# Optimization experiments

Hardware: AMD Instinct MI355X
Metric: run time of the kernel (lower is better)

## Reference

```python
import jax, jax.numpy as jnp
import numpy as np
import math

D = 1024
H = 16
HD = D // H


def setup_inputs() -> dict:
    key = jax.random.key(0)
    ks = jax.random.split(key, 12)
    B, L = 2, 2048
    s = 1.0 / math.sqrt(D)
    inp = {
        "q": jax.random.normal(ks[0], (B, L, D), jnp.float32),
        "k": jax.random.normal(ks[1], (B, L, D), jnp.float32),
        "v": jax.random.normal(ks[2], (B, L, D), jnp.float32),
        "Wq": jax.random.normal(ks[3], (D, D), jnp.float32) * s,
        "bq": jnp.zeros((D,), jnp.float32),
        "Wk": jax.random.normal(ks[4], (D, D), jnp.float32) * s,
        "bk": jnp.zeros((D,), jnp.float32),
        "Wv": jax.random.normal(ks[5], (D, D), jnp.float32) * s,
        "bv": jnp.zeros((D,), jnp.float32),
        "Wo": jax.random.normal(ks[6], (D, D), jnp.float32) * s,
        "bo": jnp.zeros((D,), jnp.float32),
        "P": jax.random.normal(ks[7], (H, H), jnp.float32),  # logit_proj_pre
    }
    return inp


def _split_heads(x, B, L):
    # [B,L,D] -> [B,H,L,HD]
    return x.reshape(B, L, H, HD).transpose(0, 2, 1, 3)


def reference(q, k, v, Wq, bq, Wk, bk, Wv, bv, Wo, bo, P):
    B, L, _ = q.shape
    qh = _split_heads(q @ Wq.T + bq, B, L)
    kh = _split_heads(k @ Wk.T + bk, B, L)
    vh = _split_heads(v @ Wv.T + bv, B, L)
    # raw per-head logits [B,H,L,L]
    logits = jnp.einsum("bhld,bhmd->bhlm", qh, kh) / math.sqrt(HD)
    # talking-heads mixing across heads (pre-softmax)
    logits = jnp.einsum("bhlm,hg->bglm", logits, P)
    attn = jax.nn.softmax(logits, axis=-1)
    out = jnp.einsum("bhlm,bhmd->bhld", attn, vh)  # [B,H,L,HD]
    out = out.transpose(0, 2, 1, 3).reshape(B, L, D)
    return out @ Wo.T + bo
```

## Files before the change

kernel.cpp:

```cpp
#include <hip/hip_runtime.h>

#define D_  1024
#define H_  16
#define HD_ 64
#define L_  2048
#define B_  2
#define M_  (B_*L_)

typedef float f32x4  __attribute__((ext_vector_type(4)));
typedef short bf16x4 __attribute__((ext_vector_type(4)));
typedef short bf16x8 __attribute__((ext_vector_type(8)));

#define SRAW_PITCH 18
#define SRAW_SLAB  (16 * SRAW_PITCH)
#define VS_PITCH   36

__device__ __forceinline__ float bf2f(short s) {
    return __uint_as_float(((unsigned int)(unsigned short)s) << 16);
}
__device__ __forceinline__ short f2bf(float f) {
    unsigned u = __float_as_uint(f);
    unsigned r = (u + 0x7FFFu + ((u >> 16) & 1u)) >> 16;
    return (short)r;
}
__device__ __forceinline__ void block_sync() {
    asm volatile("s_waitcnt lgkmcnt(0)" ::: "memory");
    __builtin_amdgcn_sched_barrier(0);
    __builtin_amdgcn_s_barrier();
    __builtin_amdgcn_sched_barrier(0);
}

__global__ __launch_bounds__(256) void proj_mfma(
    const float* __restrict__ q, const float* __restrict__ k, const float* __restrict__ v,
    const float* __restrict__ Wq, const float* __restrict__ bq,
    const float* __restrict__ Wk, const float* __restrict__ bk,
    const float* __restrict__ Wv, const float* __restrict__ bv,
    short* __restrict__ qh, short* __restrict__ qlo,
    short* __restrict__ kh, short* __restrict__ vht)
{
    const int z = blockIdx.z;
    const float* X    = (z == 0) ? q  : (z == 1) ? k  : v;
    const float* W    = (z == 0) ? Wq : (z == 1) ? Wk : Wv;
    const float* bias = (z == 0) ? bq : (z == 1) ? bk : bv;

    __shared__ short Ws[128][40];
    __shared__ short Xs[128][40];

    const int tid  = threadIdx.x;
    const int w    = tid >> 6, lane = tid & 63;
    const int l16  = lane & 15, qq = lane >> 4;
    const int m0   = blockIdx.x * 128;
    const int n0   = blockIdx.y * 128;
    const int ar0  = 64 * (w & 1);
    const int br0  = 64 * (w >> 1);

    f32x4 acc[4][4] = {};

    for (int k0 = 0; k0 < D_; k0 += 32) {
        #pragma unroll
        for (int i = 0; i < 4; ++i) {
            int fidx = i * 256 + tid;
            int r = fidx >> 3, c = fidx & 7;
            float4 wv4 = *(const float4*)(W + (size_t)(n0 + r) * D_ + k0 + c * 4);
            float4 xv4 = *(const float4*)(X + (size_t)(m0 + r) * D_ + k0 + c * 4);
            bf16x4 wb = { f2bf(wv4.x), f2bf(wv4.y), f2bf(wv4.z), f2bf(wv4.w) };
            bf16x4 xb = { f2bf(xv4.x), f2bf(xv4.y), f2bf(xv4.z), f2bf(xv4.w) };
            *(bf16x4*)&Ws[r][c * 4] = wb;
            *(bf16x4*)&Xs[r][c * 4] = xb;
        }
        __syncthreads();
        bf16x8 af[4], bfv[4];
        #pragma unroll
        for (int i = 0; i < 4; ++i) {
            const short* Ab = (z < 2) ? &Ws[ar0 + 16 * i + l16][qq * 8]
                                      : &Xs[ar0 + 16 * i + l16][qq * 8];
            const short* Bb = (z < 2) ? &Xs[br0 + 16 * i + l16][qq * 8]
                                      : &Ws[br0 + 16 * i + l16][qq * 8];
            af[i]  = *(const bf16x8*)Ab;
            bfv[i] = *(const bf16x8*)Bb;
        }
        #pragma unroll
        for (int i = 0; i < 4; ++i)
            #pragma unroll
            for (int j = 0; j < 4; ++j)
                acc[i][j] = __builtin_amdgcn_mfma_f32_16x16x32_bf16(af[i], bfv[j], acc[i][j], 0, 0, 0);
        __syncthreads();
    }

    if (z < 2) {
        #pragma unroll
        for (int i = 0; i < 4; ++i) {
            int nb = n0 + ar0 + 16 * i + qq * 4;
            float4 b4 = *(const float4*)(bias + nb);
            int h = nb >> 6, hd = nb & 63;
            #pragma unroll
            for (int j = 0; j < 4; ++j) {
                int m = m0 + br0 + 16 * j + l16;
                int bb = m >> 11, l = m & (L_ - 1);
                size_t o = ((((size_t)bb * H_ + h) * L_) + l) * HD_ + hd;
                f32x4 c = acc[i][j];
                float v0 = c[0] + b4.x, v1 = c[1] + b4.y, v2 = c[2] + b4.z, v3 = c[3] + b4.w;
                bf16x4 hi = { f2bf(v0), f2bf(v1), f2bf(v2), f2bf(v3) };
                if (z == 0) {
                    *(bf16x4*)&qh[o] = hi;
                    bf16x4 lo = { f2bf(v0 - bf2f(hi[0])), f2bf(v1 - bf2f(hi[1])),
                                  f2bf(v2 - bf2f(hi[2])), f2bf(v3 - bf2f(hi[3])) };
                    *(bf16x4*)&qlo[o] = lo;
                } else {
                    *(bf16x4*)&kh[o] = hi;
                }
            }
        }
    } else {
        #pragma unroll
        for (int i = 0; i < 4; ++i) {
            int mb = m0 + ar0 + 16 * i + qq * 4;
            int bb = mb >> 11, lb = mb & (L_ - 1);
            #pragma unroll
            for (int j = 0; j < 4; ++j) {
                int n = n0 + br0 + 16 * j + l16;
                int h = n >> 6, hd = n & 63;
                float bn = bias[n];
                size_t o = (((size_t)bb * H_ + h) * HD_ + hd) * (size_t)L_ + lb;
                f32x4 c = acc[i][j];
                bf16x4 ov = { f2bf(c[0] + bn), f2bf(c[1] + bn), f2bf(c[2] + bn), f2bf(c[3] + bn) };
                *(bf16x4*)&vht[o] = ov;
            }
        }
    }
}

__global__ __launch_bounds__(512, 2) void attn_mfma(
    const short* __restrict__ qh, const short* __restrict__ qlo,
    const short* __restrict__ kh, const short* __restrict__ vht,
    const float* __restrict__ P, short* __restrict__ attn_out)
{
    __shared__ __align__(16) float Sraw0[16 * SRAW_SLAB];
    __shared__ __align__(16) float Sraw1[16 * SRAW_SLAB];
    __shared__ __align__(16) float Smix[16 * SRAW_SLAB];
    __shared__ __align__(16) short Vslab[8][2 * 64 * VS_PITCH];
    __shared__ float PmS[256];

    const int tid  = threadIdx.x;
    const int n    = blockIdx.x;
    const int b    = (n >> 2) & 1;
    const int l0   = ((n >> 3) * 4 + (n & 3)) * 16;
    const int w    = tid >> 6, lane = tid & 63;
    const int l16  = lane & 15, qq = lane >> 4;
    const size_t hb = (size_t)b * H_;

    bf16x8 qf[2][2][2];
    #pragma unroll
    for (int hh = 0; hh < 2; ++hh)
        #pragma unroll
        for (int kc = 0; kc < 2; ++kc) {
            size_t off = ((hb + 2 * w + hh) * L_ + l0 + l16) * HD_ + kc * 32 + qq * 8;
            qf[hh][kc][0] = *(const bf16x8*)(qh  + off);
            qf[hh][kc][1] = *(const bf16x8*)(qlo + off);
        }

    int vgi_[4], vd_[4];
    const int vc = lane & 1;
    #pragma unroll
    for (int i = 0; i < 4; ++i) {
        int vrow = i * 32 + (lane >> 1);
        vgi_[i] = vrow >> 6;
        vd_[i]  = vrow & 63;
    }
    int vwoff[4];
    #pragma unroll
    for (int i = 0; i < 4; ++i)
        vwoff[i] = vgi_[i] * (64 * VS_PITCH) + vd_[i] * VS_PITCH + vc * 8;

    bf16x8 kA[2][2], kB[2][2], vA[4], vB[4];
    #pragma unroll
    for (int hh = 0; hh < 2; ++hh)
        #pragma unroll
        for (int kc = 0; kc < 2; ++kc) {
            kA[hh][kc] = *(const bf16x8*)(kh + ((hb + 2 * w + hh) * L_ + 0  + l16) * HD_ + kc * 32 + qq * 8);
            kB[hh][kc] = *(const bf16x8*)(kh + ((hb + 2 * w + hh) * L_ + 16 + l16) * HD_ + kc * 32 + qq * 8);
        }
    #pragma unroll
    for (int i = 0; i < 4; ++i) {
        vA[i] = *(const bf16x8*)(vht + ((hb + 2 * w + vgi_[i]) * HD_ + vd_[i]) * (size_t)L_ + 0  + vc * 8);
        vB[i] = *(const bf16x8*)(vht + ((hb + 2 * w + vgi_[i]) * HD_ + vd_[i]) * (size_t)L_ + 16 + vc * 8);
    }

    if (tid < 256) PmS[tid] = P[tid] * 0.125f;

    f32x4 acc[2][4];
    #pragma unroll
    for (int dt = 0; dt < 4; ++dt) { acc[0][dt] = (f32x4){0.f,0.f,0.f,0.f}; acc[1][dt] = (f32x4){0.f,0.f,0.f,0.f}; }
    float mrun0 = 0.f, mrun1 = 0.f, srun0 = 0.f, srun1 = 0.f;

    auto qkt = [&](bf16x8 (&kr)[2][2], float* sb) {
        #pragma unroll
        for (int hh = 0; hh < 2; ++hh) {
            f32x4 s = (f32x4){0.f,0.f,0.f,0.f};
            s = __builtin_amdgcn_mfma_f32_16x16x32_bf16(kr[hh][0], qf[hh][0][0], s, 0, 0, 0);
            s = __builtin_amdgcn_mfma_f32_16x16x32_bf16(kr[hh][0], qf[hh][0][1], s, 0, 0, 0);
            s = __builtin_amdgcn_mfma_f32_16x16x32_bf16(kr[hh][1], qf[hh][1][0], s, 0, 0, 0);
            s = __builtin_amdgcn_mfma_f32_16x16x32_bf16(kr[hh][1], qf[hh][1][1], s, 0, 0, 0);
            float* sp = sb + ((2 * w + hh) * 16 + l16) * SRAW_PITCH + qq * 4;
            *(float2*)sp       = make_float2(s[0], s[1]);
            *(float2*)(sp + 2) = make_float2(s[2], s[3]);
        }
    };

    qkt(kA, Sraw0);
    block_sync();

    bf16x4 PAhi, PAlo;
    {
        float p0 = PmS[(qq * 4 + 0) * 16 + l16];
        float p1 = PmS[(qq * 4 + 1) * 16 + l16];
        float p2 = PmS[(qq * 4 + 2) * 16 + l16];
        float p3 = PmS[(qq * 4 + 3) * 16 + l16];
        PAhi = (bf16x4){ f2bf(p0), f2bf(p1), f2bf(p2), f2bf(p3) };
        PAlo = (bf16x4){ f2bf(p0 - bf2f(PAhi[0])), f2bf(p1 - bf2f(PAhi[1])),
                         f2bf(p2 - bf2f(PAhi[2])), f2bf(p3 - bf2f(PAhi[3])) };
    }

    auto mixmfma = [&](const float* sb) {
        #pragma unroll
        for (int mi = 0; mi < 2; ++mi) {
            const int m = 2 * w + mi;
            float sv0 = sb[(qq * 4 + 0) * SRAW_SLAB + l16 * SRAW_PITCH + m];
            float sv1 = sb[(qq * 4 + 1) * SRAW_SLAB + l16 * SRAW_PITCH + m];
            float sv2 = sb[(qq * 4 + 2) * SRAW_SLAB + l16 * SRAW_PITCH + m];
            float sv3 = sb[(qq * 4 + 3) * SRAW_SLAB + l16 * SRAW_PITCH + m];
            bf16x4 bhi = { f2bf(sv0), f2bf(sv1), f2bf(sv2), f2bf(sv3) };
            bf16x4 blo = { f2bf(sv0 - bf2f(bhi[0])), f2bf(sv1 - bf2f(bhi[1])),
                           f2bf(sv2 - bf2f(bhi[2])), f2bf(sv3 - bf2f(bhi[3])) };
            f32x4 c = (f32x4){0.f, 0.f, 0.f, 0.f};
            c = __builtin_amdgcn_mfma_f32_16x16x16bf16_1k(PAhi, bhi, c, 0, 0, 0);
            c = __builtin_amdgcn_mfma_f32_16x16x16bf16_1k(PAhi, blo, c, 0, 0, 0);
            c = __builtin_amdgcn_mfma_f32_16x16x16bf16_1k(PAlo, bhi, c, 0, 0, 0);
            float* sp = Smix + m * SRAW_SLAB + l16 * SRAW_PITCH + qq * 4;
            *(float2*)sp       = make_float2(c[0], c[1]);
            *(float2*)(sp + 2) = make_float2(c[2], c[3]);
        }
    };

    auto body = [&](const float* sb, float* sbo, bf16x8 (&vstage)[4], bf16x8 (&kqk)[2][2],
                    bf16x8 (&kld)[2][2], bf16x8 (&vld)[4], int tnext) {
        #pragma unroll
        for (int i = 0; i < 4; ++i) {
            bf16x4 wlo = { vstage[i][0], vstage[i][1], vstage[i][2], vstage[i][3] };
            bf16x4 whi = { vstage[i][4], vstage[i][5], vstage[i][6], vstage[i][7] };
            *(bf16x4*)&Vslab[w][vwoff[i]]     = wlo;
            *(bf16x4*)&Vslab[w][vwoff[i] + 4] = whi;
        }
        {
            const int mn = tnext * 16;
            #pragma unroll
            for (int hh = 0; hh < 2; ++hh)
                #pragma unroll
                for (int kc = 0; kc < 2; ++kc)
                    kld[hh][kc] = *(const bf16x8*)(kh + ((hb + 2 * w + hh) * L_ + mn + l16) * HD_ + kc * 32 + qq * 8);
            #pragma unroll
            for (int i = 0; i < 4; ++i)
                vld[i] = *(const bf16x8*)(vht + ((hb + 2 * w + vgi_[i]) * HD_ + vd_[i]) * (size_t)L_ + mn + vc * 8);
        }
        mixmfma(sb);
        block_sync();
        float sx0[4], sx1[4];
        #pragma unroll
        for (int j = 0; j < 4; ++j) {
            const float* mp = Smix + (qq * 4 + j) * SRAW_SLAB + l16 * SRAW_PITCH;
            sx0[j] = mp[2 * w];
            sx1[j] = mp[2 * w + 1];
        }
        float e00 = __expf(sx0[0] - mrun0), e01 = __expf(sx0[1] - mrun0);
        float e02 = __expf(sx0[2] - mrun0), e03 = __expf(sx0[3] - mrun0);
        float e10 = __expf(sx1[0] - mrun1), e11 = __expf(sx1[1] - mrun1);
        float e12 = __expf(sx1[2] - mrun1), e13 = __expf(sx1[3] - mrun1);
        bf16x4 pf0 = { f2bf(e00), f2bf(e01), f2bf(e02), f2bf(e03) };
        bf16x4 pf1 = { f2bf(e10), f2bf(e11), f2bf(e12), f2bf(e13) };
        float t0 = fmaxf(fmaxf(sx0[0], sx0[1]), fmaxf(sx0[2], sx0[3]));
        float t1 = fmaxf(fmaxf(sx1[0], sx1[1]), fmaxf(sx1[2], sx1[3]));
        t0 = fmaxf(t0, __shfl_xor(t0, 16)); t0 = fmaxf(t0, __shfl_xor(t0, 32));
        t1 = fmaxf(t1, __shfl_xor(t1, 16)); t1 = fmaxf(t1, __shfl_xor(t1, 32));
        float ps0 = e00 + e01 + e02 + e03, ps1 = e10 + e11 + e12 + e13;
        ps0 += __shfl_xor(ps0, 16); ps0 += __shfl_xor(ps0, 32);
        ps1 += __shfl_xor(ps1, 16); ps1 += __shfl_xor(ps1, 32);
        #pragma unroll
        for (int i = 0; i < 2; ++i) {
            bf16x4 pf = i ? pf1 : pf0;
            #pragma unroll
            for (int dt = 0; dt < 4; ++dt) {
                bf16x4 afr = *(const bf16x4*)&Vslab[w][i * (64 * VS_PITCH) + (dt * 16 + l16) * VS_PITCH + qq * 4];
                acc[i][dt] = __builtin_amdgcn_mfma_f32_16x16x16bf16_1k(afr, pf, acc[i][dt], 0, 0, 0);
            }
        }
        qkt(kqk, sbo);
        float mnew0 = fmaxf(mrun0, t0), mnew1 = fmaxf(mrun1, t1);
        float corr0 = __expf(mrun0 - mnew0), corr1 = __expf(mrun1 - mnew1);
        srun0 = (srun0 + ps0) * corr0; srun1 = (srun1 + ps1) * corr1;
        acc[0][0] *= corr0; acc[0][1] *= corr0; acc[0][2] *= corr0; acc[0][3] *= corr0;
        acc[1][0] *= corr1; acc[1][1] *= corr1; acc[1][2] *= corr1; acc[1][3] *= corr1;
        mrun0 = mnew0; mrun1 = mnew1;
        block_sync();
    };

    for (int itp = 0; itp < 64; ++itp) {
        const int t0 = 2 * itp;
        body(Sraw0, Sraw1, vA, kB, kA, vA, (t0 + 2) & 127);
        body(Sraw1, Sraw0, vB, kA, kB, vB, (t0 + 3) & 127);
    }

    float inv0 = 1.f / srun0, inv1 = 1.f / srun1;
    #pragma unroll
    for (int i = 0; i < 2; ++i) {
        float inv = i ? inv1 : inv0;
        #pragma unroll
        for (int dt = 0; dt < 4; ++dt) {
            f32x4 a = acc[i][dt];
            bf16x4 ov = { f2bf(a[0] * inv), f2bf(a[1] * inv), f2bf(a[2] * inv), f2bf(a[3] * inv) };
            *(bf16x4*)(attn_out + ((size_t)(b * L_ + l0 + l16)) * D_ + (2 * w + i) * 64 + dt * 16 + qq * 4) = ov;
        }
    }
}

__global__ __launch_bounds__(256) void out_mfma(
    const short* __restrict__ attn, const float* __restrict__ Wo,
    const float* __restrict__ bo, float* __restrict__ out)
{
    __shared__ short Ws[128][40];
    __shared__ short Xs[128][40];

    const int tid = threadIdx.x;
    const int w = tid >> 6, lane = tid & 63;
    const int l16 = lane & 15, qq = lane >> 4;
    const int m0 = blockIdx.x * 128;
    const int n0 = blockIdx.y * 128;
    const int ar0 = 64 * (w & 1);
    const int br0 = 64 * (w >> 1);

    f32x4 acc[4][4] = {};

    for (int k0 = 0; k0 < D_; k0 += 32) {
        #pragma unroll
        for (int i = 0; i < 4; ++i) {
            int fidx = i * 256 + tid;
            int r = fidx >> 3, c = fidx & 7;
            float4 wv4 = *(const float4*)(Wo + (size_t)(n0 + r) * D_ + k0 + c * 4);
            bf16x4 wb = { f2bf(wv4.x), f2bf(wv4.y), f2bf(wv4.z), f2bf(wv4.w) };
            *(bf16x4*)&Ws[r][c * 4] = wb;
        }
        #pragma unroll
        for (int i = 0; i < 2; ++i) {
            int cidx = i * 256 + tid;
            int r = cidx >> 2, c = cidx & 3;
            bf16x8 xv = *(const bf16x8*)(attn + (size_t)(m0 + r) * D_ + k0 + c * 8);
            *(bf16x8*)&Xs[r][c * 8] = xv;
        }
        __syncthreads();
        bf16x8 af[4], bfv[4];
        #pragma unroll
        for (int i = 0; i < 4; ++i) {
            af[i]  = *(const bf16x8*)&Ws[ar0 + 16 * i + l16][qq * 8];
            bfv[i] = *(const bf16x8*)&Xs[br0 + 16 * i + l16][qq * 8];
        }
        #pragma unroll
        for (int i = 0; i < 4; ++i)
            #pragma unroll
            for (int j = 0; j < 4; ++j)
                acc[i][j] = __builtin_amdgcn_mfma_f32_16x16x32_bf16(af[i], bfv[j], acc[i][j], 0, 0, 0);
        __syncthreads();
    }

    #pragma unroll
    for (int i = 0; i < 4; ++i) {
        int nb = n0 + ar0 + 16 * i + qq * 4;
        float4 b4 = *(const float4*)(bo + nb);
        #pragma unroll
        for (int j = 0; j < 4; ++j) {
            int m = m0 + br0 + 16 * j + l16;
            f32x4 c = acc[i][j];
            float4 ov = make_float4(c[0] + b4.x, c[1] + b4.y, c[2] + b4.z, c[3] + b4.w);
            *(float4*)&out[(size_t)m * D_ + nb] = ov;
        }
    }
}

extern "C" void kernel_launch(void* const* d_in, const int* in_sizes, int n_in,
                              void* d_out, int out_size, void* d_ws, size_t ws_size,
                              hipStream_t stream) {
    const float* q  = (const float*)d_in[0];
    const float* k  = (const float*)d_in[1];
    const float* v  = (const float*)d_in[2];
    const float* Wq = (const float*)d_in[3];
    const float* bq = (const float*)d_in[4];
    const float* Wk = (const float*)d_in[5];
    const float* bk = (const float*)d_in[6];
    const float* Wv = (const float*)d_in[7];
    const float* bv = (const float*)d_in[8];
    const float* Wo = (const float*)d_in[9];
    const float* bo = (const float*)d_in[10];
    const float* P  = (const float*)d_in[11];
    float* out = (float*)d_out;

    char* ws = (char*)d_ws;
    short* qh   = (short*)(ws);
    short* qlo  = (short*)(ws + (size_t)8 * 1024 * 1024);
    short* kh   = (short*)(ws + (size_t)16 * 1024 * 1024);
    short* vht  = (short*)(ws + (size_t)24 * 1024 * 1024);
    short* attn = (short*)(ws + (size_t)32 * 1024 * 1024);

    proj_mfma<<<dim3(M_ / 128, D_ / 128, 3), 256, 0, stream>>>(
        q, k, v, Wq, bq, Wk, bk, Wv, bv, qh, qlo, kh, vht);
    attn_mfma<<<dim3(256), 512, 0, stream>>>(qh, qlo, kh, vht, P, attn);
    out_mfma<<<dim3(M_ / 128, D_ / 128), 256, 0, stream>>>(attn, Wo, bo, out);
}
```

Measured before the change: 408.1 us.

## Process two key tiles per attention iteration to halve block barriers

The attention loop now handles two 16-key tiles per iteration. A second Smix buffer lets both tiles be head-mixed before a single barrier, and one online-softmax max/sum update covers both tiles. K and V fragments are prefetched two tiles ahead through small load lambdas. This halves the number of block-wide barriers and exposes more independent MFMA/exp work, at the cost of extra LDS (another Smix slab) and higher register pressure.

```diff
diff --git a/kernel.cpp b/kernel.cpp
--- a/kernel.cpp
+++ b/kernel.cpp
@@ -135,9 +135,10 @@
     const short* __restrict__ kh, const short* __restrict__ vht,
     const float* __restrict__ P, short* __restrict__ attn_out)
 {
-    __shared__ __align__(16) float Sraw0[16 * SRAW_SLAB];
-    __shared__ __align__(16) float Sraw1[16 * SRAW_SLAB];
-    __shared__ __align__(16) float Smix[16 * SRAW_SLAB];
+    __shared__ __align__(16) float SrawA[16 * SRAW_SLAB];
+    __shared__ __align__(16) float SrawB[16 * SRAW_SLAB];
+    __shared__ __align__(16) float SmixA[16 * SRAW_SLAB];
+    __shared__ __align__(16) float SmixB[16 * SRAW_SLAB];
     __shared__ __align__(16) short Vslab[8][2 * 64 * VS_PITCH];
     __shared__ float PmS[256];
 
@@ -172,19 +173,24 @@
     for (int i = 0; i < 4; ++i)
         vwoff[i] = vgi_[i] * (64 * VS_PITCH) + vd_[i] * VS_PITCH + vc * 8;
 
-    bf16x8 kA[2][2], kB[2][2], vA[4], vB[4];
-    #pragma unroll
-    for (int hh = 0; hh < 2; ++hh)
-        #pragma unroll
-        for (int kc = 0; kc < 2; ++kc) {
-            kA[hh][kc] = *(const bf16x8*)(kh + ((hb + 2 * w + hh) * L_ + 0  + l16) * HD_ + kc * 32 + qq * 8);
-            kB[hh][kc] = *(const bf16x8*)(kh + ((hb + 2 * w + hh) * L_ + 16 + l16) * HD_ + kc * 32 + qq * 8);
-        }
-    #pragma unroll
-    for (int i = 0; i < 4; ++i) {
-        vA[i] = *(const bf16x8*)(vht + ((hb + 2 * w + vgi_[i]) * HD_ + vd_[i]) * (size_t)L_ + 0  + vc * 8);
-        vB[i] = *(const bf16x8*)(vht + ((hb + 2 * w + vgi_[i]) * HD_ + vd_[i]) * (size_t)L_ + 16 + vc * 8);
-    }
+    auto kload = [&](int tile, bf16x8 (&kdst)[2][2]) {
+        const int mn = (tile & 127) * 16;
+        #pragma unroll
+        for (int hh = 0; hh < 2; ++hh)
+            #pragma unroll
+            for (int kc = 0; kc < 2; ++kc)
+                kdst[hh][kc] = *(const bf16x8*)(kh + ((hb + 2 * w + hh) * L_ + mn + l16) * HD_ + kc * 32 + qq * 8);
+    };
+    auto vload = [&](int tile, bf16x8 (&vdst)[4]) {
+        const int mn = (tile & 127) * 16;
+        #pragma unroll
+        for (int i = 0; i < 4; ++i)
+            vdst[i] = *(const bf16x8*)(vht + ((hb + 2 * w + vgi_[i]) * HD_ + vd_[i]) * (size_t)L_ + mn + vc * 8);
+    };
+
+    bf16x8 kPa[2][2], kPb[2][2], vsta[4], vstb[4];
+    kload(0, kPa); kload(1, kPb);
+    vload(0, vsta); vload(1, vstb);
 
     if (tid < 256) PmS[tid] = P[tid] * 0.125f;
 
@@ -207,8 +213,10 @@
         }
     };
 
-    qkt(kA, Sraw0);
+    qkt(kPa, SrawA);
+    qkt(kPb, SrawB);
     block_sync();
+    kload(2, kPa); kload(3, kPb);
 
     bf16x4 PAhi, PAlo;
     {
@@ -221,7 +229,7 @@
                          f2bf(p2 - bf2f(PAhi[2])), f2bf(p3 - bf2f(PAhi[3])) };
     }
 
-    auto mixmfma = [&](const float* sb) {
+    auto mixmfma = [&](const float* sb, float* sm) {
         #pragma unroll
         for (int mi = 0; mi < 2; ++mi) {
             const int m = 2 * w + mi;
@@ -236,54 +244,20 @@
             c = __builtin_amdgcn_mfma_f32_16x16x16bf16_1k(PAhi, bhi, c, 0, 0, 0);
             c = __builtin_amdgcn_mfma_f32_16x16x16bf16_1k(PAhi, blo, c, 0, 0, 0);
             c = __builtin_amdgcn_mfma_f32_16x16x16bf16_1k(PAlo, bhi, c, 0, 0, 0);
-            float* sp = Smix + m * SRAW_SLAB + l16 * SRAW_PITCH + qq * 4;
+            float* sp = sm + m * SRAW_SLAB + l16 * SRAW_PITCH + qq * 4;
             *(float2*)sp       = make_float2(c[0], c[1]);
             *(float2*)(sp + 2) = make_float2(c[2], c[3]);
         }
     };
 
-    auto body = [&](const float* sb, float* sbo, bf16x8 (&vstage)[4], bf16x8 (&kqk)[2][2],
-                    bf16x8 (&kld)[2][2], bf16x8 (&vld)[4], int tnext) {
-        #pragma unroll
-        for (int i = 0; i < 4; ++i) {
-            bf16x4 wlo = { vstage[i][0], vstage[i][1], vstage[i][2], vstage[i][3] };
-            bf16x4 whi = { vstage[i][4], vstage[i][5], vstage[i][6], vstage[i][7] };
+    auto stage_pv = [&](bf16x8 (&vst)[4], bf16x4 pf0, bf16x4 pf1) {
+        #pragma unroll
+        for (int i = 0; i < 4; ++i) {
+            bf16x4 wlo = { vst[i][0], vst[i][1], vst[i][2], vst[i][3] };
+            bf16x4 whi = { vst[i][4], vst[i][5], vst[i][6], vst[i][7] };
             *(bf16x4*)&Vslab[w][vwoff[i]]     = wlo;
             *(bf16x4*)&Vslab[w][vwoff[i] + 4] = whi;
         }
-        {
-            const int mn = tnext * 16;
-            #pragma unroll
-            for (int hh = 0; hh < 2; ++hh)
-                #pragma unroll
-                for (int kc = 0; kc < 2; ++kc)
-                    kld[hh][kc] = *(const bf16x8*)(kh + ((hb + 2 * w + hh) * L_ + mn + l16) * HD_ + kc * 32 + qq * 8);
-            #pragma unroll
-            for (int i = 0; i < 4; ++i)
-                vld[i] = *(const bf16x8*)(vht + ((hb + 2 * w + vgi_[i]) * HD_ + vd_[i]) * (size_t)L_ + mn + vc * 8);
-        }
-        mixmfma(sb);
-        block_sync();
-        float sx0[4], sx1[4];
-        #pragma unroll
-        for (int j = 0; j < 4; ++j) {
-            const float* mp = Smix + (qq * 4 + j) * SRAW_SLAB + l16 * SRAW_PITCH;
-            sx0[j] = mp[2 * w];
-            sx1[j] = mp[2 * w + 1];
-        }
-        float e00 = __expf(sx0[0] - mrun0), e01 = __expf(sx0[1] - mrun0);
-        float e02 = __expf(sx0[2] - mrun0), e03 = __expf(sx0[3] - mrun0);
-        float e10 = __expf(sx1[0] - mrun1), e11 = __expf(sx1[1] - mrun1);
-        float e12 = __expf(sx1[2] - mrun1), e13 = __expf(sx1[3] - mrun1);
-        bf16x4 pf0 = { f2bf(e00), f2bf(e01), f2bf(e02), f2bf(e03) };
-        bf16x4 pf1 = { f2bf(e10), f2bf(e11), f2bf(e12), f2bf(e13) };
-        float t0 = fmaxf(fmaxf(sx0[0], sx0[1]), fmaxf(sx0[2], sx0[3]));
-        float t1 = fmaxf(fmaxf(sx1[0], sx1[1]), fmaxf(sx1[2], sx1[3]));
-        t0 = fmaxf(t0, __shfl_xor(t0, 16)); t0 = fmaxf(t0, __shfl_xor(t0, 32));
-        t1 = fmaxf(t1, __shfl_xor(t1, 16)); t1 = fmaxf(t1, __shfl_xor(t1, 32));
-        float ps0 = e00 + e01 + e02 + e03, ps1 = e10 + e11 + e12 + e13;
-        ps0 += __shfl_xor(ps0, 16); ps0 += __shfl_xor(ps0, 32);
-        ps1 += __shfl_xor(ps1, 16); ps1 += __shfl_xor(ps1, 32);
         #pragma unroll
         for (int i = 0; i < 2; ++i) {
             bf16x4 pf = i ? pf1 : pf0;
@@ -293,7 +267,50 @@
                 acc[i][dt] = __builtin_amdgcn_mfma_f32_16x16x16bf16_1k(afr, pf, acc[i][dt], 0, 0, 0);
             }
         }
-        qkt(kqk, sbo);
+    };
+
+    for (int t = 0; t < 64; ++t) {
+        mixmfma(SrawA, SmixA);
+        mixmfma(SrawB, SmixB);
+        block_sync();
+        float sxA0[4], sxA1[4], sxB0[4], sxB1[4];
+        #pragma unroll
+        for (int j = 0; j < 4; ++j) {
+            const float* mpA = SmixA + (qq * 4 + j) * SRAW_SLAB + l16 * SRAW_PITCH;
+            const float* mpB = SmixB + (qq * 4 + j) * SRAW_SLAB + l16 * SRAW_PITCH;
+            sxA0[j] = mpA[2 * w]; sxA1[j] = mpA[2 * w + 1];
+            sxB0[j] = mpB[2 * w]; sxB1[j] = mpB[2 * w + 1];
+        }
+        float eA00 = __expf(sxA0[0] - mrun0), eA01 = __expf(sxA0[1] - mrun0);
+        float eA02 = __expf(sxA0[2] - mrun0), eA03 = __expf(sxA0[3] - mrun0);
+        float eA10 = __expf(sxA1[0] - mrun1), eA11 = __expf(sxA1[1] - mrun1);
+        float eA12 = __expf(sxA1[2] - mrun1), eA13 = __expf(sxA1[3] - mrun1);
+        float eB00 = __expf(sxB0[0] - mrun0), eB01 = __expf(sxB0[1] - mrun0);
+        float eB02 = __expf(sxB0[2] - mrun0), eB03 = __expf(sxB0[3] - mrun0);
+        float eB10 = __expf(sxB1[0] - mrun1), eB11 = __expf(sxB1[1] - mrun1);
+        float eB12 = __expf(sxB1[2] - mrun1), eB13 = __expf(sxB1[3] - mrun1);
+        bf16x4 pfA0 = { f2bf(eA00), f2bf(eA01), f2bf(eA02), f2bf(eA03) };
+        bf16x4 pfA1 = { f2bf(eA10), f2bf(eA11), f2bf(eA12), f2bf(eA13) };
+        bf16x4 pfB0 = { f2bf(eB00), f2bf(eB01), f2bf(eB02), f2bf(eB03) };
+        bf16x4 pfB1 = { f2bf(eB10), f2bf(eB11), f2bf(eB12), f2bf(eB13) };
+        float t0 = fmaxf(fmaxf(fmaxf(sxA0[0], sxA0[1]), fmaxf(sxA0[2], sxA0[3])),
+                         fmaxf(fmaxf(sxB0[0], sxB0[1]), fmaxf(sxB0[2], sxB0[3])));
+        float t1 = fmaxf(fmaxf(fmaxf(sxA1[0], sxA1[1]), fmaxf(sxA1[2], sxA1[3])),
+                         fmaxf(fmaxf(sxB1[0], sxB1[1]), fmaxf(sxB1[2], sxB1[3])));
+        t0 = fmaxf(t0, __shfl_xor(t0, 16)); t0 = fmaxf(t0, __shfl_xor(t0, 32));
+        t1 = fmaxf(t1, __shfl_xor(t1, 16)); t1 = fmaxf(t1, __shfl_xor(t1, 32));
+        float ps0 = (eA00 + eA01 + eA02 + eA03) + (eB00 + eB01 + eB02 + eB03);
+        float ps1 = (eA10 + eA11 + eA12 + eA13) + (eB10 + eB11 + eB12 + eB13);
+        ps0 += __shfl_xor(ps0, 16); ps0 += __shfl_xor(ps0, 32);
+        ps1 += __shfl_xor(ps1, 16); ps1 += __shfl_xor(ps1, 32);
+        stage_pv(vsta, pfA0, pfA1);
+        vload(2 * t + 2, vsta);
+        stage_pv(vstb, pfB0, pfB1);
+        vload(2 * t + 3, vstb);
+        qkt(kPa, SrawA);
+        qkt(kPb, SrawB);
+        kload(2 * t + 4, kPa);
+        kload(2 * t + 5, kPb);
         float mnew0 = fmaxf(mrun0, t0), mnew1 = fmaxf(mrun1, t1);
         float corr0 = __expf(mrun0 - mnew0), corr1 = __expf(mrun1 - mnew1);
         srun0 = (srun0 + ps0) * corr0; srun1 = (srun1 + ps1) * corr1;
@@ -301,12 +318,6 @@
         acc[1][0] *= corr1; acc[1][1] *= corr1; acc[1][2] *= corr1; acc[1][3] *= corr1;
         mrun0 = mnew0; mrun1 = mnew1;
         block_sync();
-    };
-
-    for (int itp = 0; itp < 64; ++itp) {
-        const int t0 = 2 * itp;
-        body(Sraw0, Sraw1, vA, kB, kA, vA, (t0 + 2) & 127);
-        body(Sraw1, Sraw0, vB, kA, kB, vB, (t0 + 3) & 127);
     }
 
     float inv0 = 1.f / srun0, inv1 = 1.f / srun1;
```

Measured after the change: 403.9 us. Within noise of the previous version (-1.0%).

## Split attention KV range across two blocks and merge partial softmax results

Applied to the files above, without the earlier changes.

The attention kernel now splits the 2048-key range into two halves, so twice as many blocks (512) are launched, each handling 64 tiles. Each block writes fp32 partial accumulators and running max/sum to workspace, and a new merge kernel combines them with a log-sum-exp rescale. The main loop is restructured around a single Sraw buffer, with K/V prefetch reordered and a smaller V slab pitch, and the occupancy hint is raised to 4 blocks. The aim is better CU occupancy across the GPU, at the cost of extra global traffic for partials and one more launch; it falls back to the old path if the workspace is too small.

```diff
diff --git a/kernel.cpp b/kernel.cpp
--- a/kernel.cpp
+++ b/kernel.cpp
@@ -13,7 +13,7 @@
 
 #define SRAW_PITCH 18
 #define SRAW_SLAB  (16 * SRAW_PITCH)
-#define VS_PITCH   36
+#define VS_PITCH   20
 
 __device__ __forceinline__ float bf2f(short s) {
     return __uint_as_float(((unsigned int)(unsigned short)s) << 16);
@@ -130,21 +130,24 @@
     }
 }
 
-__global__ __launch_bounds__(512, 2) void attn_mfma(
+__global__ __launch_bounds__(512, 4) void attn_mfma(
     const short* __restrict__ qh, const short* __restrict__ qlo,
     const short* __restrict__ kh, const short* __restrict__ vht,
-    const float* __restrict__ P, short* __restrict__ attn_out)
+    const float* __restrict__ P, short* __restrict__ attn_out,
+    float* __restrict__ pacc, float* __restrict__ pms, int ntiles)
 {
-    __shared__ __align__(16) float Sraw0[16 * SRAW_SLAB];
-    __shared__ __align__(16) float Sraw1[16 * SRAW_SLAB];
+    __shared__ __align__(16) float Sraw[16 * SRAW_SLAB];
     __shared__ __align__(16) float Smix[16 * SRAW_SLAB];
     __shared__ __align__(16) short Vslab[8][2 * 64 * VS_PITCH];
     __shared__ float PmS[256];
 
     const int tid  = threadIdx.x;
     const int n    = blockIdx.x;
-    const int b    = (n >> 2) & 1;
-    const int l0   = ((n >> 3) * 4 + (n & 3)) * 16;
+    const int half = n >> 8;
+    const int inr  = n & 255;
+    const int b    = (inr >> 2) & 1;
+    const int l0   = ((inr >> 3) * 4 + (inr & 3)) * 16;
+    const int tb   = half * ntiles;
     const int w    = tid >> 6, lane = tid & 63;
     const int l16  = lane & 15, qq = lane >> 4;
     const size_t hb = (size_t)b * H_;
@@ -172,19 +175,23 @@
     for (int i = 0; i < 4; ++i)
         vwoff[i] = vgi_[i] * (64 * VS_PITCH) + vd_[i] * VS_PITCH + vc * 8;
 
-    bf16x8 kA[2][2], kB[2][2], vA[4], vB[4];
-    #pragma unroll
-    for (int hh = 0; hh < 2; ++hh)
-        #pragma unroll
-        for (int kc = 0; kc < 2; ++kc) {
-            kA[hh][kc] = *(const bf16x8*)(kh + ((hb + 2 * w + hh) * L_ + 0  + l16) * HD_ + kc * 32 + qq * 8);
-            kB[hh][kc] = *(const bf16x8*)(kh + ((hb + 2 * w + hh) * L_ + 16 + l16) * HD_ + kc * 32 + qq * 8);
-        }
-    #pragma unroll
-    for (int i = 0; i < 4; ++i) {
-        vA[i] = *(const bf16x8*)(vht + ((hb + 2 * w + vgi_[i]) * HD_ + vd_[i]) * (size_t)L_ + 0  + vc * 8);
-        vB[i] = *(const bf16x8*)(vht + ((hb + 2 * w + vgi_[i]) * HD_ + vd_[i]) * (size_t)L_ + 16 + vc * 8);
-    }
+    auto kload = [&](int tile, bf16x8 (&kdst)[2][2]) {
+        const int mn = (tile & 127) * 16;
+        #pragma unroll
+        for (int hh = 0; hh < 2; ++hh)
+            #pragma unroll
+            for (int kc = 0; kc < 2; ++kc)
+                kdst[hh][kc] = *(const bf16x8*)(kh + ((hb + 2 * w + hh) * L_ + mn + l16) * HD_ + kc * 32 + qq * 8);
+    };
+    auto vload = [&](int tile, bf16x8 (&vdst)[4]) {
+        const int mn = (tile & 127) * 16;
+        #pragma unroll
+        for (int i = 0; i < 4; ++i)
+            vdst[i] = *(const bf16x8*)(vht + ((hb + 2 * w + vgi_[i]) * HD_ + vd_[i]) * (size_t)L_ + mn + vc * 8);
+    };
+
+    bf16x8 kP[2][2], vst[4];
+    kload(tb, kP); vload(tb, vst);
 
     if (tid < 256) PmS[tid] = P[tid] * 0.125f;
 
@@ -207,8 +214,9 @@
         }
     };
 
-    qkt(kA, Sraw0);
+    qkt(kP, Sraw);
     block_sync();
+    kload(tb + 1, kP);
 
     bf16x4 PAhi, PAlo;
     {
@@ -221,14 +229,14 @@
                          f2bf(p2 - bf2f(PAhi[2])), f2bf(p3 - bf2f(PAhi[3])) };
     }
 
-    auto mixmfma = [&](const float* sb) {
+    for (int t = 0; t < ntiles; ++t) {
         #pragma unroll
         for (int mi = 0; mi < 2; ++mi) {
             const int m = 2 * w + mi;
-            float sv0 = sb[(qq * 4 + 0) * SRAW_SLAB + l16 * SRAW_PITCH + m];
-            float sv1 = sb[(qq * 4 + 1) * SRAW_SLAB + l16 * SRAW_PITCH + m];
-            float sv2 = sb[(qq * 4 + 2) * SRAW_SLAB + l16 * SRAW_PITCH + m];
-            float sv3 = sb[(qq * 4 + 3) * SRAW_SLAB + l16 * SRAW_PITCH + m];
+            float sv0 = Sraw[(qq * 4 + 0) * SRAW_SLAB + l16 * SRAW_PITCH + m];
+            float sv1 = Sraw[(qq * 4 + 1) * SRAW_SLAB + l16 * SRAW_PITCH + m];
+            float sv2 = Sraw[(qq * 4 + 2) * SRAW_SLAB + l16 * SRAW_PITCH + m];
+            float sv3 = Sraw[(qq * 4 + 3) * SRAW_SLAB + l16 * SRAW_PITCH + m];
             bf16x4 bhi = { f2bf(sv0), f2bf(sv1), f2bf(sv2), f2bf(sv3) };
             bf16x4 blo = { f2bf(sv0 - bf2f(bhi[0])), f2bf(sv1 - bf2f(bhi[1])),
                            f2bf(sv2 - bf2f(bhi[2])), f2bf(sv3 - bf2f(bhi[3])) };
@@ -240,30 +248,9 @@
             *(float2*)sp       = make_float2(c[0], c[1]);
             *(float2*)(sp + 2) = make_float2(c[2], c[3]);
         }
-    };
-
-    auto body = [&](const float* sb, float* sbo, bf16x8 (&vstage)[4], bf16x8 (&kqk)[2][2],
-                    bf16x8 (&kld)[2][2], bf16x8 (&vld)[4], int tnext) {
-        #pragma unroll
-        for (int i = 0; i < 4; ++i) {
-            bf16x4 wlo = { vstage[i][0], vstage[i][1], vstage[i][2], vstage[i][3] };
-            bf16x4 whi = { vstage[i][4], vstage[i][5], vstage[i][6], vstage[i][7] };
-            *(bf16x4*)&Vslab[w][vwoff[i]]     = wlo;
-            *(bf16x4*)&Vslab[w][vwoff[i] + 4] = whi;
-        }
-        {
-            const int mn = tnext * 16;
-            #pragma unroll
-            for (int hh = 0; hh < 2; ++hh)
-                #pragma unroll
-                for (int kc = 0; kc < 2; ++kc)
-                    kld[hh][kc] = *(const bf16x8*)(kh + ((hb + 2 * w + hh) * L_ + mn + l16) * HD_ + kc * 32 + qq * 8);
-            #pragma unroll
-            for (int i = 0; i < 4; ++i)
-                vld[i] = *(const bf16x8*)(vht + ((hb + 2 * w + vgi_[i]) * HD_ + vd_[i]) * (size_t)L_ + mn + vc * 8);
-        }
-        mixmfma(sb);
         block_sync();
+        qkt(kP, Sraw);
+        kload(tb + t + 2, kP);
         float sx0[4], sx1[4];
         #pragma unroll
         for (int j = 0; j < 4; ++j) {
@@ -277,13 +264,20 @@
         float e12 = __expf(sx1[2] - mrun1), e13 = __expf(sx1[3] - mrun1);
         bf16x4 pf0 = { f2bf(e00), f2bf(e01), f2bf(e02), f2bf(e03) };
         bf16x4 pf1 = { f2bf(e10), f2bf(e11), f2bf(e12), f2bf(e13) };
-        float t0 = fmaxf(fmaxf(sx0[0], sx0[1]), fmaxf(sx0[2], sx0[3]));
-        float t1 = fmaxf(fmaxf(sx1[0], sx1[1]), fmaxf(sx1[2], sx1[3]));
-        t0 = fmaxf(t0, __shfl_xor(t0, 16)); t0 = fmaxf(t0, __shfl_xor(t0, 32));
-        t1 = fmaxf(t1, __shfl_xor(t1, 16)); t1 = fmaxf(t1, __shfl_xor(t1, 32));
+        float t0r = fmaxf(fmaxf(sx0[0], sx0[1]), fmaxf(sx0[2], sx0[3]));
+        float t1r = fmaxf(fmaxf(sx1[0], sx1[1]), fmaxf(sx1[2], sx1[3]));
+        t0r = fmaxf(t0r, __shfl_xor(t0r, 16)); t0r = fmaxf(t0r, __shfl_xor(t0r, 32));
+        t1r = fmaxf(t1r, __shfl_xor(t1r, 16)); t1r = fmaxf(t1r, __shfl_xor(t1r, 32));
         float ps0 = e00 + e01 + e02 + e03, ps1 = e10 + e11 + e12 + e13;
         ps0 += __shfl_xor(ps0, 16); ps0 += __shfl_xor(ps0, 32);
         ps1 += __shfl_xor(ps1, 16); ps1 += __shfl_xor(ps1, 32);
+        #pragma unroll
+        for (int i = 0; i < 4; ++i) {
+            bf16x4 wlo = { vst[i][0], vst[i][1], vst[i][2], vst[i][3] };
+            bf16x4 whi = { vst[i][4], vst[i][5], vst[i][6], vst[i][7] };
+            *(bf16x4*)&Vslab[w][vwoff[i]]     = wlo;
+            *(bf16x4*)&Vslab[w][vwoff[i] + 4] = whi;
+        }
         #pragma unroll
         for (int i = 0; i < 2; ++i) {
             bf16x4 pf = i ? pf1 : pf0;
@@ -293,33 +287,67 @@
                 acc[i][dt] = __builtin_amdgcn_mfma_f32_16x16x16bf16_1k(afr, pf, acc[i][dt], 0, 0, 0);
             }
         }
-        qkt(kqk, sbo);
-        float mnew0 = fmaxf(mrun0, t0), mnew1 = fmaxf(mrun1, t1);
+        vload(tb + t + 1, vst);
+        float mnew0 = fmaxf(mrun0, t0r), mnew1 = fmaxf(mrun1, t1r);
         float corr0 = __expf(mrun0 - mnew0), corr1 = __expf(mrun1 - mnew1);
         srun0 = (srun0 + ps0) * corr0; srun1 = (srun1 + ps1) * corr1;
         acc[0][0] *= corr0; acc[0][1] *= corr0; acc[0][2] *= corr0; acc[0][3] *= corr0;
         acc[1][0] *= corr1; acc[1][1] *= corr1; acc[1][2] *= corr1; acc[1][3] *= corr1;
         mrun0 = mnew0; mrun1 = mnew1;
         block_sync();
-    };
-
-    for (int itp = 0; itp < 64; ++itp) {
-        const int t0 = 2 * itp;
-        body(Sraw0, Sraw1, vA, kB, kA, vA, (t0 + 2) & 127);
-        body(Sraw1, Sraw0, vB, kA, kB, vB, (t0 + 3) & 127);
-    }
-
-    float inv0 = 1.f / srun0, inv1 = 1.f / srun1;
-    #pragma unroll
-    for (int i = 0; i < 2; ++i) {
-        float inv = i ? inv1 : inv0;
-        #pragma unroll
-        for (int dt = 0; dt < 4; ++dt) {
-            f32x4 a = acc[i][dt];
-            bf16x4 ov = { f2bf(a[0] * inv), f2bf(a[1] * inv), f2bf(a[2] * inv), f2bf(a[3] * inv) };
-            *(bf16x4*)(attn_out + ((size_t)(b * L_ + l0 + l16)) * D_ + (2 * w + i) * 64 + dt * 16 + qq * 4) = ov;
-        }
-    }
+    }
+
+    if (pacc) {
+        #pragma unroll
+        for (int i = 0; i < 2; ++i) {
+            int g = 2 * w + i;
+            #pragma unroll
+            for (int dt = 0; dt < 4; ++dt)
+                *(f32x4*)&pacc[(((size_t)n * 16 + g) * 16 + l16) * 64 + dt * 16 + qq * 4] = acc[i][dt];
+        }
+        if (qq == 0) {
+            *(float2*)&pms[(((size_t)n * 16 + 2 * w)     * 16 + l16) * 2] = make_float2(mrun0, srun0);
+            *(float2*)&pms[(((size_t)n * 16 + 2 * w + 1) * 16 + l16) * 2] = make_float2(mrun1, srun1);
+        }
+    } else {
+        float inv0 = 1.f / srun0, inv1 = 1.f / srun1;
+        #pragma unroll
+        for (int i = 0; i < 2; ++i) {
+            float inv = i ? inv1 : inv0;
+            #pragma unroll
+            for (int dt = 0; dt < 4; ++dt) {
+                f32x4 a = acc[i][dt];
+                bf16x4 ov = { f2bf(a[0] * inv), f2bf(a[1] * inv), f2bf(a[2] * inv), f2bf(a[3] * inv) };
+                *(bf16x4*)(attn_out + ((size_t)(b * L_ + l0 + l16)) * D_ + (2 * w + i) * 64 + dt * 16 + qq * 4) = ov;
+            }
+        }
+    }
+}
+
+__global__ __launch_bounds__(256) void merge_attn(
+    const float* __restrict__ pacc, const float* __restrict__ pms,
+    short* __restrict__ attn)
+{
+    const int cid = blockIdx.x * 256 + threadIdx.x;
+    const int d4 = cid & 15;
+    const int g  = (cid >> 4) & 15;
+    const int l  = (cid >> 8) & (L_ - 1);
+    const int b  = cid >> 19;
+    const int lt = l >> 4, l16 = l & 15;
+    const int n0 = ((lt >> 2) << 3) + (b << 2) + (lt & 3);
+    const int n1 = n0 + 256;
+
+    float2 ms0 = *(const float2*)&pms[(((size_t)n0 * 16 + g) * 16 + l16) * 2];
+    float2 ms1 = *(const float2*)&pms[(((size_t)n1 * 16 + g) * 16 + l16) * 2];
+    f32x4 o0 = *(const f32x4*)&pacc[(((size_t)n0 * 16 + g) * 16 + l16) * 64 + d4 * 4];
+    f32x4 o1 = *(const f32x4*)&pacc[(((size_t)n1 * 16 + g) * 16 + l16) * 64 + d4 * 4];
+    float Mx = fmaxf(ms0.x, ms1.x);
+    float w0 = __expf(ms0.x - Mx), w1 = __expf(ms1.x - Mx);
+    float s = ms0.y * w0 + ms1.y * w1;
+    float inv = 1.f / s;
+    f32x4 o = o0 * w0 + o1 * w1;
+    bf16x4 ov = { f2bf(o[0] * inv), f2bf(o[1] * inv), f2bf(o[2] * inv), f2bf(o[3] * inv) };
+    *(bf16x4*)(attn + ((size_t)(b * L_ + l) * D_) + g * 64 + d4 * 4) = ov;
 }
 
 __global__ __launch_bounds__(256) void out_mfma(
@@ -407,9 +435,20 @@
     short* kh   = (short*)(ws + (size_t)16 * 1024 * 1024);
     short* vht  = (short*)(ws + (size_t)24 * 1024 * 1024);
     short* attn = (short*)(ws + (size_t)32 * 1024 * 1024);
+    float* pacc = (float*)(ws + (size_t)40 * 1024 * 1024);
+    float* pms  = (float*)(ws + (size_t)40 * 1024 * 1024 + (size_t)512 * 16 * 16 * 64 * 4);
+    const size_t need2 = (size_t)40 * 1024 * 1024
+                       + (size_t)512 * 16 * 16 * 64 * 4
+                       + (size_t)512 * 16 * 16 * 2 * 4;
+    const bool split2 = (ws_size >= need2);
 
     proj_mfma<<<dim3(M_ / 128, D_ / 128, 3), 256, 0, stream>>>(
         q, k, v, Wq, bq, Wk, bk, Wv, bv, qh, qlo, kh, vht);
-    attn_mfma<<<dim3(256), 512, 0, stream>>>(qh, qlo, kh, vht, P, attn);
+    if (split2) {
+        attn_mfma<<<dim3(512), 512, 0, stream>>>(qh, qlo, kh, vht, P, attn, pacc, pms, 64);
+        merge_attn<<<dim3(4096), 256, 0, stream>>>(pacc, pms, attn);
+    } else {
+        attn_mfma<<<dim3(256), 512, 0, stream>>>(qh, qlo, kh, vht, P, attn, nullptr, nullptr, 128);
+    }
     out_mfma<<<dim3(M_ / 128, D_ / 128), 256, 0, stream>>>(attn, Wo, bo, out);
 }
```

Result: slower. 475.7 us (+16.6%).
